# Kernel tuning notes

Hardware: AMD Instinct MI355X
Metric: run time of the kernel (lower is better)

## Reference

```python
import jax, jax.numpy as jnp
import numpy as np

VOCAB, EMB, HID = 32000, 512, 1024


def setup_inputs() -> dict:
    key = jax.random.key(0)
    k1, k2, k3, k4, k5, k6 = jax.random.split(key, 6)
    sentences = jax.random.randint(k1, (64, 512), 0, VOCAB)
    emb_table = jax.random.normal(k2, (VOCAB, EMB), dtype=jnp.float32)
    s_ih = 1.0 / np.sqrt(HID)
    # PyTorch LSTM params: gate order (i, f, g, o)
    w_ih = jax.random.uniform(k3, (4 * HID, EMB), minval=-s_ih, maxval=s_ih, dtype=jnp.float32)
    w_hh = jax.random.uniform(k4, (4 * HID, HID), minval=-s_ih, maxval=s_ih, dtype=jnp.float32)
    b_ih = jax.random.uniform(k5, (4 * HID,), minval=-s_ih, maxval=s_ih, dtype=jnp.float32)
    b_hh = jax.random.uniform(k6, (4 * HID,), minval=-s_ih, maxval=s_ih, dtype=jnp.float32)
    return {"sentences": sentences, "emb_table": emb_table,
            "w_ih": w_ih, "w_hh": w_hh, "b_ih": b_ih, "b_hh": b_hh}


def _lstm_forward(emb_table, w_ih, w_hh, b_ih, b_hh, sentences):
    B = sentences.shape[0]
    H = w_hh.shape[1]
    # embedding lookup -> [T, B, E] (matches transpose(0,1) in torch code)
    embedded = emb_table[sentences].transpose(1, 0, 2)
    # precompute input projections for all timesteps: [T, B, 4H]
    x_gates = jnp.einsum('tbe,ge->tbg', embedded, w_ih) + b_ih + b_hh

    def step(carry, xg):
        h, c = carry
        gates = xg + h @ w_hh.T  # [B, 4H]
        i, f, g, o = jnp.split(gates, 4, axis=-1)
        i = jax.nn.sigmoid(i)
        f = jax.nn.sigmoid(f)
        g = jnp.tanh(g)
        o = jax.nn.sigmoid(o)
        c_new = f * c + i * g
        h_new = o * jnp.tanh(c_new)
        return (h_new, c_new), None

    h0 = jnp.zeros((B, H), dtype=emb_table.dtype)
    c0 = jnp.zeros((B, H), dtype=emb_table.dtype)
    (h, c), _ = jax.lax.scan(step, (h0, c0), x_gates)
    # original returns output of last step only: [1, B, H], and (h, c) each [1, B, H]
    return h[None], (h[None], c[None])


def reference(sentences, emb_table, w_ih, w_hh, b_ih, b_hh):
    output, (h, c) = _lstm_forward(emb_table, w_ih, w_hh, b_ih, b_hh, sentences)
    return output, h, c
```

## Files before the change

### kernel.cpp

```cpp
#include <hip/hip_runtime.h>

typedef __bf16 bf16x8 __attribute__((ext_vector_type(8)));
typedef float f32x4 __attribute__((ext_vector_type(4)));
typedef unsigned short u16;
typedef unsigned long long u64;

#define NSTEP 512

#define AL(p)   __hip_atomic_load((p), __ATOMIC_RELAXED, __HIP_MEMORY_SCOPE_AGENT)
#define AS(p,v) __hip_atomic_store((p), (v), __ATOMIC_RELAXED, __HIP_MEMORY_SCOPE_AGENT)

__device__ __forceinline__ u16 f2bf(float f) {
  union { float f; unsigned u; } x; x.f = f;
  return (u16)((x.u + 0x7fffu + ((x.u >> 16) & 1u)) >> 16);
}

__global__ void prep_kernel(u64* __restrict__ H0, int* __restrict__ F) {
  int i = blockIdx.x * blockDim.x + threadIdx.x;
  if (i < 16384) AS(H0 + i, 0ULL);
  if (i < 32768) AS(&F[i], 0);
}

__global__ void gather_kernel(const int* __restrict__ sent, const float* __restrict__ emb,
                              u16* __restrict__ A1) {
  int row = blockIdx.x * 4 + (threadIdx.x >> 6);
  int lane = threadIdx.x & 63;
  int t = row >> 6, b = row & 63;
  int idx = sent[b * 512 + t];
  const float* src = emb + (size_t)idx * 512 + lane * 8;
  u16* dst = A1 + (size_t)row * 512 + lane * 8;
  #pragma unroll
  for (int k = 0; k < 8; ++k) dst[k] = f2bf(src[k]);
}

__global__ void __launch_bounds__(256, 2)
lstm_kernel(const u16* __restrict__ A1,
            const float* __restrict__ wih, const float* __restrict__ whh,
            const float* __restrict__ bih, const float* __restrict__ bhh,
            u16* __restrict__ H, float* __restrict__ out, int* __restrict__ F) {
  __shared__ u16 wlds[48 * 16 * 36];
  __shared__ alignas(8) u16 hx[4][16][4];

  const int j   = blockIdx.x;
  const int tid = threadIdx.x;
  const int w   = tid >> 6;
  const int l   = tid & 63;
  const int lr  = l & 15, lk = l >> 4;
  const int g   = lr >> 2, nn = lr & 3;
  const int wrow = g * 1024 + j * 4 + nn;

  for (int task = tid; task < 3072; task += 256) {
    int kk = task >> 6;
    int rem = task & 63;
    int rb = rem >> 2, q = rem & 3;
    int row = (rb >> 2) * 1024 + j * 4 + (rb & 3);
    const float* src = (kk < 16) ? (wih + (size_t)row * 512 + kk * 32 + q * 8)
                                 : (whh + (size_t)row * 1024 + (kk - 16) * 32 + q * 8);
    u16* dst = wlds + (kk * 16 + rb) * 36 + q * 8;
    #pragma unroll
    for (int e = 0; e < 8; ++e) dst[e] = f2bf(src[e]);
  }
  __syncthreads();

  const float bias = bih[wrow] + bhh[wrow];
  const float sca = (g == 2) ? 2.f : 1.f;
  const float bd  = (g == 2) ? -1.f : 0.f;
  const int arow = w * 16 + lr;
  const u16* bx = wlds + lr * 36 + lk * 8;

  float cst[4] = {0.f, 0.f, 0.f, 0.f};

  bf16x8 ax[16];
  {
    const u16* apre = A1 + (size_t)arow * 512 + lk * 8;
    #pragma unroll
    for (int kk = 0; kk < 16; ++kk) ax[kk] = *(const bf16x8*)(apre + kk * 32);
  }

  union AF { bf16x8 v; u64 q[2]; };

#define FADDR(c) (F + (((c) * 64 + l) * 128) + w * 32)
#define WAITV(vv, c)                                                        \
  { while (vv < t) { __builtin_amdgcn_s_sleep(1); vv = AL(FADDR(c)); } }
#define LD8(BUF, CH)                                                        \
  { _Pragma("unroll")                                                       \
    for (int r = 0; r < 8; ++r)                                             \
      BUF[r].v = *(const bf16x8*)(hp + (CH) * 256 + r * 32); }
#define MM8(BUF, W0)                                                        \
  { _Pragma("unroll")                                                       \
    for (int r = 0; r < 8; ++r) {                                           \
      bf16x8 b = *(const bf16x8*)(bx + ((W0) + r) * 576);                   \
      acc = __builtin_amdgcn_mfma_f32_16x16x32_bf16(BUF[r].v, b, acc, 0, 0, 0); \
    } }

  #pragma unroll 1
  for (int t = 0; t < NSTEP; ++t) {
    AF ha[8], hb[8];
    const u16* hp = H + (size_t)t * 65536 + (size_t)arow * 1024 + lk * 8;
    int v0 = AL(FADDR(0));
    int v1 = AL(FADDR(1));
    int v2 = AL(FADDR(2));
    int v3 = AL(FADDR(3));
    f32x4 acc = { bias, bias, bias, bias };
    #pragma unroll
    for (int kk = 0; kk < 16; ++kk) {
      bf16x8 b = *(const bf16x8*)(bx + kk * 576);
      acc = __builtin_amdgcn_mfma_f32_16x16x32_bf16(ax[kk], b, acc, 0, 0, 0);
    }
    WAITV(v0, 0);
    LD8(ha, 0);
    WAITV(v1, 1);
    LD8(hb, 1);
    MM8(ha, 16);
    WAITV(v2, 2);
    LD8(ha, 2);
    MM8(hb, 24);
    WAITV(v3, 3);
    LD8(hb, 3);
    MM8(ha, 32);
    MM8(hb, 40);

    float hv4[4], cn4[4];
    #pragma unroll
    for (int r = 0; r < 4; ++r) {
      float xv = acc[r];
      float act = sca / (1.f + __expf(-sca * xv)) + bd;
      float gg = __shfl_xor(act, 8);
      float ff = __shfl_xor(act, 4);
      float oo = __shfl_xor(act, 12);
      float cn = ff * cst[r] + act * gg;
      cst[r] = cn;
      float tc = 2.f / (1.f + __expf(-2.f * cn)) - 1.f;
      hv4[r] = oo * tc;
      cn4[r] = cn;
    }

    if (t == NSTEP - 1) {
      if (lr < 4) {
        #pragma unroll
        for (int r = 0; r < 4; ++r) {
          int R = w * 16 + lk * 4 + r;
          out[(size_t)R * 1024 + j * 4 + lr]          = hv4[r];
          out[65536 + (size_t)R * 1024 + j * 4 + lr]  = hv4[r];
          out[131072 + (size_t)R * 1024 + j * 4 + lr] = cn4[r];
        }
      }
    } else {
      if (lr < 4) {
        #pragma unroll
        for (int r = 0; r < 4; ++r) hx[w][lk * 4 + r][lr] = f2bf(hv4[r]);
      }
      if (l < 16) {
        u64 pk = *(const u64*)(&hx[w][l][0]);
        u16* hw = H + (size_t)(t + 1) * 65536 + (size_t)(w * 16 + l) * 1024 + j * 4;
        AS((u64*)hw, pk);
      }
      asm volatile("s_waitcnt vmcnt(0)" ::: "memory");
      if (l == 0) AS(F + j * 128 + w * 32, t + 1);
      {
        const u16* apre = A1 + ((size_t)(t + 1) * 64 + arow) * 512 + lk * 8;
        #pragma unroll
        for (int kk = 0; kk < 16; ++kk) ax[kk] = *(const bf16x8*)(apre + kk * 32);
      }
    }
  }
#undef FADDR
#undef WAITV
#undef LD8
#undef MM8
}

extern "C" void kernel_launch(void* const* d_in, const int* in_sizes, int n_in,
                              void* d_out, int out_size, void* d_ws, size_t ws_size,
                              hipStream_t stream) {
  const int*   sent = (const int*)d_in[0];
  const float* emb  = (const float*)d_in[1];
  const float* w_ih = (const float*)d_in[2];
  const float* w_hh = (const float*)d_in[3];
  const float* b_ih = (const float*)d_in[4];
  const float* b_hh = (const float*)d_in[5];
  float* out = (float*)d_out;

  char* ws = (char*)d_ws;
  u16* A1 = (u16*)ws;
  u16* H  = (u16*)(ws + 33554432);
  int* F  = (int*)(ws + 33554432 + 67108864);

  prep_kernel<<<256, 256, 0, stream>>>((u64*)H, F);
  gather_kernel<<<8192, 256, 0, stream>>>(sent, emb, A1);

  void* args[] = { (void*)&A1, (void*)&w_ih, (void*)&w_hh,
                   (void*)&b_ih, (void*)&b_hh, (void*)&H, (void*)&out, (void*)&F };
  hipError_t err = hipLaunchCooperativeKernel((void*)lstm_kernel, dim3(256), dim3(256),
                                              args, 0, stream);
  if (err != hipSuccess) {
    lstm_kernel<<<dim3(256), dim3(256), 0, stream>>>(A1, w_ih, w_hh, b_ih, b_hh,
                                                     H, out, F);
  }
}
```

Measured before the change: 4.272 ms.

## Halve LSTM block count, each block owns eight hidden units with dynamic LDS

Reworks the persistent cooperative LSTM kernel to run 128 blocks instead of 256. Each block now computes eight hidden columns (two 16x16 MFMA tiles) and holds twice the weights in dynamic shared memory. The aim is to halve the number of producer flags each consumer polls per step, reuse every loaded h fragment across two MFMAs, and split the input-projection MFMAs around the first wait. In exchange, half the CUs sit idle and each block does twice the MFMA and elementwise work per step, which lengthens the serial critical path.

```diff
diff --git a/kernel.cpp b/kernel.cpp
--- a/kernel.cpp
+++ b/kernel.cpp
@@ -6,6 +6,7 @@
 typedef unsigned long long u64;
 
 #define NSTEP 512
+#define WLDS_BYTES 110592
 
 #define AL(p)   __hip_atomic_load((p), __ATOMIC_RELAXED, __HIP_MEMORY_SCOPE_AGENT)
 #define AS(p,v) __hip_atomic_store((p), (v), __ATOMIC_RELAXED, __HIP_MEMORY_SCOPE_AGENT)
@@ -18,7 +19,7 @@
 __global__ void prep_kernel(u64* __restrict__ H0, int* __restrict__ F) {
   int i = blockIdx.x * blockDim.x + threadIdx.x;
   if (i < 16384) AS(H0 + i, 0ULL);
-  if (i < 32768) AS(&F[i], 0);
+  if (i < 16384) AS(&F[i], 0);
 }
 
 __global__ void gather_kernel(const int* __restrict__ sent, const float* __restrict__ emb,
@@ -33,42 +34,46 @@
   for (int k = 0; k < 8; ++k) dst[k] = f2bf(src[k]);
 }
 
-__global__ void __launch_bounds__(256, 2)
+__global__ void __launch_bounds__(256, 1)
 lstm_kernel(const u16* __restrict__ A1,
             const float* __restrict__ wih, const float* __restrict__ whh,
             const float* __restrict__ bih, const float* __restrict__ bhh,
             u16* __restrict__ H, float* __restrict__ out, int* __restrict__ F) {
-  __shared__ u16 wlds[48 * 16 * 36];
-  __shared__ alignas(8) u16 hx[4][16][4];
-
-  const int j   = blockIdx.x;
+  extern __shared__ u16 wlds[];
+  __shared__ alignas(16) u16 hx[4][16][8];
+
+  const int jc  = blockIdx.x;
   const int tid = threadIdx.x;
   const int w   = tid >> 6;
   const int l   = tid & 63;
   const int lr  = l & 15, lk = l >> 4;
   const int g   = lr >> 2, nn = lr & 3;
-  const int wrow = g * 1024 + j * 4 + nn;
-
-  for (int task = tid; task < 3072; task += 256) {
-    int kk = task >> 6;
-    int rem = task & 63;
-    int rb = rem >> 2, q = rem & 3;
-    int row = (rb >> 2) * 1024 + j * 4 + (rb & 3);
+
+  for (int task = tid; task < 6144; task += 256) {
+    int kk = task >> 7;
+    int rem = task & 127;
+    int ntt = rem >> 6;
+    int rem2 = rem & 63;
+    int rb = rem2 >> 2, q = rem2 & 3;
+    int row = (rb >> 2) * 1024 + jc * 8 + ntt * 4 + (rb & 3);
     const float* src = (kk < 16) ? (wih + (size_t)row * 512 + kk * 32 + q * 8)
                                  : (whh + (size_t)row * 1024 + (kk - 16) * 32 + q * 8);
-    u16* dst = wlds + (kk * 16 + rb) * 36 + q * 8;
+    u16* dst = wlds + (size_t)((kk * 2 + ntt) * 16 + rb) * 36 + q * 8;
     #pragma unroll
     for (int e = 0; e < 8; ++e) dst[e] = f2bf(src[e]);
   }
   __syncthreads();
 
-  const float bias = bih[wrow] + bhh[wrow];
+  const int wr0 = g * 1024 + jc * 8 + nn;
+  const int wr1 = wr0 + 4;
+  const float bias0 = bih[wr0] + bhh[wr0];
+  const float bias1 = bih[wr1] + bhh[wr1];
   const float sca = (g == 2) ? 2.f : 1.f;
   const float bd  = (g == 2) ? -1.f : 0.f;
   const int arow = w * 16 + lr;
-  const u16* bx = wlds + lr * 36 + lk * 8;
-
-  float cst[4] = {0.f, 0.f, 0.f, 0.f};
+  const u16* bxp = wlds + (size_t)lr * 36 + lk * 8;
+
+  float cst0[4] = {0,0,0,0}, cst1[4] = {0,0,0,0};
 
   bf16x8 ax[16];
   {
@@ -77,62 +82,67 @@
     for (int kk = 0; kk < 16; ++kk) ax[kk] = *(const bf16x8*)(apre + kk * 32);
   }
 
-  union AF { bf16x8 v; u64 q[2]; };
-
-#define FADDR(c) (F + (((c) * 64 + l) * 128) + w * 32)
-#define WAITV(vv, c)                                                        \
-  { while (vv < t) { __builtin_amdgcn_s_sleep(1); vv = AL(FADDR(c)); } }
+  bf16x8 ha[8], hb[8];
+
+#define WAITV(vv, P0)                                                       \
+  { while (vv < t) { __builtin_amdgcn_s_sleep(1);                           \
+                     vv = AL(F + (((P0) + l) * 4 + w) * 32); } }
 #define LD8(BUF, CH)                                                        \
   { _Pragma("unroll")                                                       \
     for (int r = 0; r < 8; ++r)                                             \
-      BUF[r].v = *(const bf16x8*)(hp + (CH) * 256 + r * 32); }
-#define MM8(BUF, W0)                                                        \
+      BUF[r] = *(const bf16x8*)(hp + (CH) * 256 + r * 32); }
+#define MMX(KK)                                                             \
+  { bf16x8 b0 = *(const bf16x8*)(bxp + (size_t)(KK) * 1152);                \
+    bf16x8 b1 = *(const bf16x8*)(bxp + (size_t)(KK) * 1152 + 576);          \
+    acx0 = __builtin_amdgcn_mfma_f32_16x16x32_bf16(ax[KK], b0, acx0, 0, 0, 0); \
+    acx1 = __builtin_amdgcn_mfma_f32_16x16x32_bf16(ax[KK], b1, acx1, 0, 0, 0); }
+#define MMH(BUF, KK0)                                                       \
   { _Pragma("unroll")                                                       \
     for (int r = 0; r < 8; ++r) {                                           \
-      bf16x8 b = *(const bf16x8*)(bx + ((W0) + r) * 576);                   \
-      acc = __builtin_amdgcn_mfma_f32_16x16x32_bf16(BUF[r].v, b, acc, 0, 0, 0); \
+      bf16x8 b0 = *(const bf16x8*)(bxp + (size_t)((KK0) + r) * 1152);       \
+      bf16x8 b1 = *(const bf16x8*)(bxp + (size_t)((KK0) + r) * 1152 + 576); \
+      ac0 = __builtin_amdgcn_mfma_f32_16x16x32_bf16(BUF[r], b0, ac0, 0, 0, 0); \
+      ac1 = __builtin_amdgcn_mfma_f32_16x16x32_bf16(BUF[r], b1, ac1, 0, 0, 0); \
     } }
 
   #pragma unroll 1
   for (int t = 0; t < NSTEP; ++t) {
-    AF ha[8], hb[8];
+    int v0 = AL(F + ((l)       * 4 + w) * 32);
+    int v1 = AL(F + ((64 + l)  * 4 + w) * 32);
+    f32x4 acx0 = { bias0, bias0, bias0, bias0 };
+    f32x4 acx1 = { bias1, bias1, bias1, bias1 };
+    #pragma unroll
+    for (int kk = 0; kk < 8; ++kk) MMX(kk);
     const u16* hp = H + (size_t)t * 65536 + (size_t)arow * 1024 + lk * 8;
-    int v0 = AL(FADDR(0));
-    int v1 = AL(FADDR(1));
-    int v2 = AL(FADDR(2));
-    int v3 = AL(FADDR(3));
-    f32x4 acc = { bias, bias, bias, bias };
-    #pragma unroll
-    for (int kk = 0; kk < 16; ++kk) {
-      bf16x8 b = *(const bf16x8*)(bx + kk * 576);
-      acc = __builtin_amdgcn_mfma_f32_16x16x32_bf16(ax[kk], b, acc, 0, 0, 0);
-    }
     WAITV(v0, 0);
     LD8(ha, 0);
-    WAITV(v1, 1);
     LD8(hb, 1);
-    MM8(ha, 16);
-    WAITV(v2, 2);
+    #pragma unroll
+    for (int kk = 8; kk < 16; ++kk) MMX(kk);
+    f32x4 ac0 = { 0.f, 0.f, 0.f, 0.f };
+    f32x4 ac1 = { 0.f, 0.f, 0.f, 0.f };
+    MMH(ha, 16);
+    WAITV(v1, 64);
     LD8(ha, 2);
-    MM8(hb, 24);
-    WAITV(v3, 3);
+    MMH(hb, 24);
     LD8(hb, 3);
-    MM8(ha, 32);
-    MM8(hb, 40);
-
-    float hv4[4], cn4[4];
+    MMH(ha, 32);
+    MMH(hb, 40);
+
+    float hv0[4], cn0[4], hv1[4], cn1[4];
     #pragma unroll
     for (int r = 0; r < 4; ++r) {
-      float xv = acc[r];
-      float act = sca / (1.f + __expf(-sca * xv)) + bd;
-      float gg = __shfl_xor(act, 8);
-      float ff = __shfl_xor(act, 4);
-      float oo = __shfl_xor(act, 12);
-      float cn = ff * cst[r] + act * gg;
-      cst[r] = cn;
-      float tc = 2.f / (1.f + __expf(-2.f * cn)) - 1.f;
-      hv4[r] = oo * tc;
-      cn4[r] = cn;
+      float x0 = acx0[r] + ac0[r];
+      float x1 = acx1[r] + ac1[r];
+      float a0 = sca / (1.f + __expf(-sca * x0)) + bd;
+      float a1 = sca / (1.f + __expf(-sca * x1)) + bd;
+      float f0 = __shfl_xor(a0, 4), g0 = __shfl_xor(a0, 8), o0 = __shfl_xor(a0, 12);
+      float f1 = __shfl_xor(a1, 4), g1 = __shfl_xor(a1, 8), o1 = __shfl_xor(a1, 12);
+      float c0 = f0 * cst0[r] + a0 * g0;
+      float c1 = f1 * cst1[r] + a1 * g1;
+      cst0[r] = c0; cst1[r] = c1;
+      hv0[r] = o0 * (2.f / (1.f + __expf(-2.f * c0)) - 1.f);  cn0[r] = c0;
+      hv1[r] = o1 * (2.f / (1.f + __expf(-2.f * c1)) - 1.f);  cn1[r] = c1;
     }
 
     if (t == NSTEP - 1) {
@@ -140,23 +150,31 @@
         #pragma unroll
         for (int r = 0; r < 4; ++r) {
           int R = w * 16 + lk * 4 + r;
-          out[(size_t)R * 1024 + j * 4 + lr]          = hv4[r];
-          out[65536 + (size_t)R * 1024 + j * 4 + lr]  = hv4[r];
-          out[131072 + (size_t)R * 1024 + j * 4 + lr] = cn4[r];
+          int C = jc * 8 + lr;
+          out[(size_t)R * 1024 + C]              = hv0[r];
+          out[65536 + (size_t)R * 1024 + C]      = hv0[r];
+          out[131072 + (size_t)R * 1024 + C]     = cn0[r];
+          out[(size_t)R * 1024 + C + 4]          = hv1[r];
+          out[65536 + (size_t)R * 1024 + C + 4]  = hv1[r];
+          out[131072 + (size_t)R * 1024 + C + 4] = cn1[r];
         }
       }
     } else {
       if (lr < 4) {
         #pragma unroll
-        for (int r = 0; r < 4; ++r) hx[w][lk * 4 + r][lr] = f2bf(hv4[r]);
+        for (int r = 0; r < 4; ++r) {
+          hx[w][lk * 4 + r][lr]     = f2bf(hv0[r]);
+          hx[w][lk * 4 + r][lr + 4] = f2bf(hv1[r]);
+        }
       }
       if (l < 16) {
-        u64 pk = *(const u64*)(&hx[w][l][0]);
-        u16* hw = H + (size_t)(t + 1) * 65536 + (size_t)(w * 16 + l) * 1024 + j * 4;
-        AS((u64*)hw, pk);
+        const u64* s = (const u64*)(&hx[w][l][0]);
+        u64* hw = (u64*)(H + (size_t)(t + 1) * 65536
+                           + (size_t)(w * 16 + l) * 1024 + jc * 8);
+        AS(hw, s[0]); AS(hw + 1, s[1]);
       }
       asm volatile("s_waitcnt vmcnt(0)" ::: "memory");
-      if (l == 0) AS(F + j * 128 + w * 32, t + 1);
+      if (l == 0) AS(F + (jc * 4 + w) * 32, t + 1);
       {
         const u16* apre = A1 + ((size_t)(t + 1) * 64 + arow) * 512 + lk * 8;
         #pragma unroll
@@ -164,10 +182,10 @@
       }
     }
   }
-#undef FADDR
 #undef WAITV
 #undef LD8
-#undef MM8
+#undef MMX
+#undef MMH
 }
 
 extern "C" void kernel_launch(void* const* d_in, const int* in_sizes, int n_in,
@@ -189,12 +207,15 @@
   prep_kernel<<<256, 256, 0, stream>>>((u64*)H, F);
   gather_kernel<<<8192, 256, 0, stream>>>(sent, emb, A1);
 
+  (void)hipFuncSetAttribute((const void*)lstm_kernel,
+                            hipFuncAttributeMaxDynamicSharedMemorySize, WLDS_BYTES);
+
   void* args[] = { (void*)&A1, (void*)&w_ih, (void*)&w_hh,
                    (void*)&b_ih, (void*)&b_hh, (void*)&H, (void*)&out, (void*)&F };
-  hipError_t err = hipLaunchCooperativeKernel((void*)lstm_kernel, dim3(256), dim3(256),
-                                              args, 0, stream);
+  hipError_t err = hipLaunchCooperativeKernel((void*)lstm_kernel, dim3(128), dim3(256),
+                                              args, WLDS_BYTES, stream);
   if (err != hipSuccess) {
-    lstm_kernel<<<dim3(256), dim3(256), 0, stream>>>(A1, w_ih, w_hh, b_ih, b_hh,
-                                                     H, out, F);
-  }
-}
+    lstm_kernel<<<dim3(128), dim3(256), WLDS_BYTES, stream>>>(A1, w_ih, w_hh,
+                                                              b_ih, b_hh, H, out, F);
+  }
+}
```

Measured after the change: 6.940 ms. 1.62x slower.
